# Kernel tuning notes

Hardware: AMD Instinct MI355X
Metric: run time of the kernel (lower is better)

Reference implementation:

```python
import jax, jax.numpy as jnp
import numpy as np

B, S, D = 2, 1024, 1024
H, KVH, HD = 16, 4, 64  # query heads, kv heads, head_dim
EPS = 1e-5
SCALE = float(np.sqrt(HD))  # note: scale uses original head_dim, not concat dim


def rmsnorm(x, g):
    return x * jax.lax.rsqrt(jnp.mean(x * x, axis=-1, keepdims=True) + EPS) * g


def rope(x, cos, sin):
    # x: [B,S,h,HD]; cos/sin: [S, HD//2]; pairs are consecutive (view_as_complex layout)
    xr = x.reshape(*x.shape[:-1], HD // 2, 2)
    x0, x1 = xr[..., 0], xr[..., 1]
    c = cos[None, :, None, :]
    s = sin[None, :, None, :]
    o0 = x0 * c - x1 * s
    o1 = x0 * s + x1 * c
    return jnp.stack([o0, o1], axis=-1).reshape(x.shape)


def context_build(x, W, gq, gk):
    comb = x @ W.T  # [B,S, H*HD + 2*KVH*HD]
    q, k, v = jnp.split(comb, [H * HD, H * HD + KVH * HD], axis=-1)
    q = rmsnorm(q, gq).reshape(B, S, H, HD)
    k = rmsnorm(k, gk).reshape(B, S, KVH, HD)
    v = v.reshape(B, S, KVH, HD)
    return q, k, v


def setup_inputs() -> dict:
    key = jax.random.key(0)
    ks = jax.random.split(key, 12)
    total = H * HD + 2 * KVH * HD  # 1536
    pos = jnp.arange(S, dtype=jnp.float32)
    theta = 10000.0 ** (-jnp.arange(0, HD, 2, dtype=jnp.float32) / HD)  # [HD//2]
    ang = pos[:, None] * theta[None, :]  # [S, HD//2]
    sc = 0.02
    return {
        "local_c": jax.random.normal(ks[0], (B, S, D), jnp.float32),
        "global_c": jax.random.normal(ks[1], (B, S, D), jnp.float32),
        "freqs_cos": jnp.cos(ang),
        "freqs_sin": jnp.sin(ang),
        "W_lc": jax.random.normal(ks[2], (total, D), jnp.float32) * sc,
        "W_gc": jax.random.normal(ks[3], (total, D), jnp.float32) * sc,
        "g_q_lc": jnp.ones((H * HD,), jnp.float32),
        "g_k_lc": jnp.ones((KVH * HD,), jnp.float32),
        "g_q_gc": jnp.ones((H * HD,), jnp.float32),
        "g_k_gc": jnp.ones((KVH * HD,), jnp.float32),
        "W_local": jax.random.normal(ks[4], (H * HD, 2 * H * HD), jnp.float32) * sc,
        "b_local": jnp.zeros((H * HD,), jnp.float32),
        "g_lc_out": jnp.ones((H * HD,), jnp.float32),
        "W_global": jax.random.normal(ks[5], (H * HD, 2 * H * HD), jnp.float32) * sc,
        "b_global": jnp.zeros((H * HD,), jnp.float32),
        "g_gc_out": jnp.ones((H * HD,), jnp.float32),
    }


def reference(local_c, global_c, freqs_cos, freqs_sin, W_lc, W_gc,
              g_q_lc, g_k_lc, g_q_gc, g_k_gc,
              W_local, b_local, g_lc_out, W_global, b_global, g_gc_out):
    q_lc, k_lc, v_lc = context_build(local_c, W_lc, g_q_lc, g_k_lc)
    q_gc, k_gc, v_gc = context_build(global_c, W_gc, g_q_gc, g_k_gc)

    q_lc = rope(q_lc, freqs_cos, freqs_sin)
    k_lc = rope(k_lc, freqs_cos, freqs_sin)
    q_gc = rope(q_gc, freqs_cos, freqs_sin)
    k_gc = rope(k_gc, freqs_cos, freqs_sin)

    # concat local+global along head_dim -> per-head dim 2*HD
    q = jnp.concatenate([q_lc, q_gc], axis=-1)  # [B,S,H,2HD]
    k = jnp.concatenate([k_lc, k_gc], axis=-1)  # [B,S,KVH,2HD]
    v = jnp.concatenate([v_lc, v_gc], axis=-1)

    n_rep = H // KVH
    k = jnp.repeat(k, n_rep, axis=2)  # [B,S,H,2HD] (GQA repeat_kv)
    v = jnp.repeat(v, n_rep, axis=2)

    scores = jnp.einsum("bqhd,bkhd->bhqk", q, k) / SCALE  # [B,H,S,S]
    attn = jax.nn.softmax(scores, axis=-1)
    out = jnp.einsum("bhqk,bkhd->bqhd", attn, v).reshape(B, S, H * 2 * HD)

    x_lc = rmsnorm(out @ W_local.T + b_local, g_lc_out)
    x_gc = rmsnorm(out @ W_global.T + b_global, g_gc_out)
    return (x_lc, x_gc)
```

## Files before the change

kernel.cpp:

```cpp
#include <hip/hip_runtime.h>

typedef __attribute__((ext_vector_type(8))) __bf16 bf16x8;
typedef __attribute__((ext_vector_type(4))) __bf16 bf16x4;
typedef __attribute__((ext_vector_type(4))) float f32x4;

__device__ __forceinline__ bf16x8 cvt8(const float* __restrict__ p)
{
    const float4 a = *(const float4*)p;
    const float4 b = *(const float4*)(p + 4);
    bf16x8 r;
    r[0] = (__bf16)a.x; r[1] = (__bf16)a.y; r[2] = (__bf16)a.z; r[3] = (__bf16)a.w;
    r[4] = (__bf16)b.x; r[5] = (__bf16)b.y; r[6] = (__bf16)b.z; r[7] = (__bf16)b.w;
    return r;
}

__device__ __forceinline__ void gld16(const __bf16* g, __bf16* l)
{
    __builtin_amdgcn_global_load_lds(
        (const __attribute__((address_space(1))) void*)g,
        (__attribute__((address_space(3))) void*)l, 16, 0, 0);
}

struct CvtArgs {
    const float* s[6];
    __bf16* d[6];
    int n[6];
};

__global__ __launch_bounds__(256) void cvt_bf16(CvtArgs a)
{
    const int t = blockIdx.y;
    const int i0 = (blockIdx.x * 256 + threadIdx.x) * 8;
    if (i0 < a.n[t])
        *(bf16x8*)(a.d[t] + i0) = cvt8(a.s[t] + i0);
}

template <typename CT>
__device__ __forceinline__ void gemm_core(const __bf16* __restrict__ Ap, int lda,
                                          const __bf16* __restrict__ Bp, int ldb,
                                          CT* __restrict__ Cp, int ldc, int K)
{
    __shared__ __bf16 As[2][128 * 32];
    __shared__ __bf16 Bs[2][128 * 32];
    const int tid  = threadIdx.x;
    const int w    = tid >> 6;
    const int lane = tid & 63;
    const int ln   = lane & 15;
    const int quad = lane >> 4;
    const int wm   = w & 1;
    const int wn   = w >> 1;

    const int srow = 32 * w + (lane >> 2);
    const int scol = (lane & 3) * 8;

    f32x4 acc[4][4];
    const f32x4 zero = {0.f, 0.f, 0.f, 0.f};
#pragma unroll
    for (int i = 0; i < 4; i++)
#pragma unroll
        for (int j = 0; j < 4; j++) acc[i][j] = zero;

    auto stage = [&](int buf, int k0) {
        gld16(Ap + (size_t)srow * lda        + k0 + scol, As[buf] + (2 * w)     * 512 + lane * 8);
        gld16(Ap + (size_t)(srow + 16) * lda + k0 + scol, As[buf] + (2 * w + 1) * 512 + lane * 8);
        gld16(Bp + (size_t)srow * ldb        + k0 + scol, Bs[buf] + (2 * w)     * 512 + lane * 8);
        gld16(Bp + (size_t)(srow + 16) * ldb + k0 + scol, Bs[buf] + (2 * w + 1) * 512 + lane * 8);
    };

    stage(0, 0);
    int buf = 0;
    for (int k0 = 0; k0 < K; k0 += 32, buf ^= 1) {
        __syncthreads();
        if (k0 + 32 < K) stage(buf ^ 1, k0 + 32);

        bf16x8 af[4], bw[4];
#pragma unroll
        for (int i = 0; i < 4; i++)
            af[i] = *(const bf16x8*)(As[buf] + (wm * 64 + i * 16 + ln) * 32 + quad * 8);
#pragma unroll
        for (int j = 0; j < 4; j++)
            bw[j] = *(const bf16x8*)(Bs[buf] + (wn * 64 + j * 16 + ln) * 32 + quad * 8);
#pragma unroll
        for (int i = 0; i < 4; i++)
#pragma unroll
            for (int j = 0; j < 4; j++)
                acc[i][j] = __builtin_amdgcn_mfma_f32_16x16x32_bf16(
                    af[i], bw[j], acc[i][j], 0, 0, 0);
    }

#pragma unroll
    for (int i = 0; i < 4; i++)
#pragma unroll
        for (int j = 0; j < 4; j++)
#pragma unroll
            for (int r = 0; r < 4; r++) {
                const int ml = wm * 64 + i * 16 + quad * 4 + r;
                const int nl = wn * 64 + j * 16 + ln;
                Cp[(size_t)ml * ldc + nl] = (CT)acc[i][j][r];
            }
}

__global__ __launch_bounds__(256) void gemm_qkv(const __bf16* __restrict__ Xbf,
                                                const __bf16* __restrict__ Wqkv,
                                                __bf16* __restrict__ comb)
{
    const int z = blockIdx.z;
    const __bf16* A = Xbf  + (size_t)z * 2048 * 1024 + (size_t)blockIdx.y * 128 * 1024;
    const __bf16* B = Wqkv + (size_t)z * 1536 * 1024 + (size_t)blockIdx.x * 128 * 1024;
    __bf16* C = comb + (size_t)z * 2048 * 1536 +
                (size_t)blockIdx.y * 128 * 1536 + (size_t)blockIdx.x * 128;
    gemm_core<__bf16>(A, 1024, B, 1024, C, 1536, 1024);
}

__global__ __launch_bounds__(256) void gemm_out(const __bf16* __restrict__ AO,
                                                const __bf16* __restrict__ Wout,
                                                __bf16* __restrict__ Y0,
                                                __bf16* __restrict__ Y1)
{
    const int kh = blockIdx.z;
    const __bf16* A = AO   + (size_t)blockIdx.y * 128 * 2048 + kh * 1024;
    const __bf16* B = Wout + (size_t)blockIdx.x * 128 * 2048 + kh * 1024;
    __bf16* Y = kh ? Y1 : Y0;
    __bf16* C = Y + (size_t)blockIdx.y * 128 * 2048 + (size_t)blockIdx.x * 128;
    gemm_core<__bf16>(A, 2048, B, 2048, C, 2048, 1024);
}

__global__ __launch_bounds__(256) void pack_qkv(
    const __bf16* __restrict__ comb,
    const float* __restrict__ fcos, const float* __restrict__ fsin,
    const float* __restrict__ g_q_lc, const float* __restrict__ g_k_lc,
    const float* __restrict__ g_q_gc, const float* __restrict__ g_k_gc,
    __bf16* __restrict__ Qb, __bf16* __restrict__ Kb, __bf16* __restrict__ Vb)
{
    const int m = blockIdx.x, ctx = blockIdx.y;
    const int b = m >> 10, s = m & 1023;
    const int tid = threadIdx.x;
    const __bf16* cr = comb + ((size_t)ctx * 2048 + m) * 1536;
    const float* gq = ctx ? g_q_gc : g_q_lc;
    const float* gk = ctx ? g_k_gc : g_k_lc;

    const bf16x4 qv = *(const bf16x4*)(cr + tid * 4);
    float sq = (float)qv[0] * (float)qv[0] + (float)qv[1] * (float)qv[1] +
               (float)qv[2] * (float)qv[2] + (float)qv[3] * (float)qv[3];
    const float kvv = (float)cr[1024 + tid];
    float sk = kvv * kvv;
#pragma unroll
    for (int off = 32; off > 0; off >>= 1) {
        sq += __shfl_down(sq, off);
        sk += __shfl_down(sk, off);
    }
    __shared__ float redq[4], redk[4];
    if ((tid & 63) == 0) { redq[tid >> 6] = sq; redk[tid >> 6] = sk; }
    __syncthreads();
    sq = redq[0] + redq[1] + redq[2] + redq[3];
    sk = redk[0] + redk[1] + redk[2] + redk[3];
    const float rq = rsqrtf(sq * (1.f / 1024.f) + 1e-5f);
    const float rk = rsqrtf(sk * (1.f / 256.f) + 1e-5f);

#pragma unroll
    for (int pp = 0; pp < 2; pp++) {
        const int p = tid + pp * 256;
        const int h = p >> 5, pi = p & 31;
        const float x0 = (float)cr[2 * p]     * rq * gq[2 * p];
        const float x1 = (float)cr[2 * p + 1] * rq * gq[2 * p + 1];
        const float c  = fcos[s * 32 + pi];
        const float sn = fsin[s * 32 + pi];
        const float o0 = (x0 * c - x1 * sn) * 0.125f;
        const float o1 = (x0 * sn + x1 * c) * 0.125f;
        const size_t qo = ((size_t)m * 16 + h) * 128 + ctx * 64 + 2 * pi;
        Qb[qo]     = (__bf16)o0;
        Qb[qo + 1] = (__bf16)o1;
    }
    if (tid < 128) {
        const int p = tid;
        const int kvh = p >> 5, pi = p & 31;
        const float x0 = (float)cr[1024 + 2 * p]     * rk * gk[2 * p];
        const float x1 = (float)cr[1024 + 2 * p + 1] * rk * gk[2 * p + 1];
        const float c  = fcos[s * 32 + pi];
        const float sn = fsin[s * 32 + pi];
        const float o0 = x0 * c - x1 * sn;
        const float o1 = x0 * sn + x1 * c;
        const size_t ko = ((size_t)(b * 4 + kvh) * 1024 + s) * 128 + ctx * 64 + 2 * pi;
        Kb[ko]     = (__bf16)o0;
        Kb[ko + 1] = (__bf16)o1;
    }
    {
        const int kvh = tid >> 6, d = tid & 63;
        Vb[((size_t)(b * 4 + kvh) * 1024 + s) * 128 + ctx * 64 + d] = cr[1280 + tid];
    }
}

__global__ __launch_bounds__(256) void v_transpose(const __bf16* __restrict__ Vb,
                                                   __bf16* __restrict__ Vtb)
{
    __shared__ __bf16 lds[64 * 64];
    const int st  = blockIdx.x;
    const int dt  = blockIdx.y;
    const int bkv = blockIdx.z;
    const int tid = threadIdx.x;
    const __bf16* src = Vb  + ((size_t)bkv * 1024 + st * 64) * 128 + dt * 64;
    __bf16*       dst = Vtb + ((size_t)bkv * 128 + dt * 64) * 1024 + st * 64;

#pragma unroll
    for (int i = 0; i < 2; i++) {
        const int c = tid + i * 256;
        const int s_in = c >> 3, ch = c & 7;
        const bf16x8 v = *(const bf16x8*)(src + (size_t)s_in * 128 + ch * 8);
        *(bf16x8*)&lds[s_in * 64 + (((ch + (s_in >> 3)) & 7) * 8)] = v;
    }
    __syncthreads();
#pragma unroll
    for (int i = 0; i < 2; i++) {
        const int c = tid + i * 256;
        const int dd = c >> 3, s0 = (c & 7) * 8;
        bf16x8 o;
#pragma unroll
        for (int jj = 0; jj < 8; jj++) {
            const int s = s0 + jj;
            o[jj] = lds[s * 64 + ((((dd >> 3) + (s >> 3)) & 7) * 8) + (dd & 7)];
        }
        *(bf16x8*)(dst + (size_t)dd * 1024 + s0) = o;
    }
}

__global__ __launch_bounds__(256) void attn(const __bf16* __restrict__ Qb,
                                            const __bf16* __restrict__ Kb,
                                            const __bf16* __restrict__ Vtb,
                                            __bf16* __restrict__ AO)
{
    __shared__ __bf16 Ks[2][64][136];
    __shared__ __bf16 Vts[2][128][72];
    __shared__ __bf16 Ps[4][16][72];

    const int tid  = threadIdx.x;
    const int w    = tid >> 6;
    const int lane = tid & 63;
    const int ln   = lane & 15;
    const int quad = lane >> 4;
    const int qt = blockIdx.x, h = blockIdx.y, b = blockIdx.z;
    const int kv = h >> 2;

    const __bf16* Kbase = Kb  + (size_t)(b * 4 + kv) * 1024 * 128;
    const __bf16* Vbase = Vtb + (size_t)(b * 4 + kv) * 128 * 1024;

    bf16x8 qf[4];
    const int qrow = qt * 64 + w * 16 + ln;
    const __bf16* qptr = Qb + ((size_t)(b * 1024 + qrow) * 16 + h) * 128;
#pragma unroll
    for (int kc = 0; kc < 4; kc++)
        qf[kc] = *(const bf16x8*)(qptr + kc * 32 + quad * 8);

    f32x4 oacc[8];
    const f32x4 zero = {0.f, 0.f, 0.f, 0.f};
#pragma unroll
    for (int j = 0; j < 8; j++) oacc[j] = zero;
    float lpart[4] = {0.f, 0.f, 0.f, 0.f};

    bf16x8 kreg[4], vreg[4];
    auto load_tiles = [&](int kt) {
        const int ks0 = kt * 64;
#pragma unroll
        for (int i = 0; i < 4; i++) {
            const int c = tid + i * 256;
            kreg[i] = *(const bf16x8*)(Kbase + (size_t)(ks0 + (c >> 4)) * 128 + (c & 15) * 8);
            vreg[i] = *(const bf16x8*)(Vbase + (size_t)(c >> 3) * 1024 + ks0 + (c & 7) * 8);
        }
    };
    auto write_tiles = [&](int buf) {
#pragma unroll
        for (int i = 0; i < 4; i++) {
            const int c = tid + i * 256;
            *(bf16x8*)&Ks[buf][c >> 4][(c & 15) * 8] = kreg[i];
            *(bf16x8*)&Vts[buf][c >> 3][(c & 7) * 8] = vreg[i];
        }
    };

    load_tiles(0);
    write_tiles(0);

    for (int kt = 0; kt < 16; kt++) {
        const int buf = kt & 1;
        if (kt + 1 < 16) load_tiles(kt + 1);
        __syncthreads();

        f32x4 sacc[4];
#pragma unroll
        for (int j = 0; j < 4; j++) {
            f32x4 a = zero;
#pragma unroll
            for (int kc = 0; kc < 4; kc++) {
                const bf16x8 kf =
                    *(const bf16x8*)&Ks[buf][j * 16 + ln][kc * 32 + quad * 8];
                a = __builtin_amdgcn_mfma_f32_16x16x32_bf16(qf[kc], kf, a, 0, 0, 0);
            }
            sacc[j] = a;
        }

#pragma unroll
        for (int j = 0; j < 4; j++)
#pragma unroll
            for (int r = 0; r < 4; r++) {
                const float p = __expf(sacc[j][r] - 20.f);
                lpart[r] += p;
                Ps[w][quad * 4 + r][j * 16 + ln] = (__bf16)p;
            }
#pragma unroll
        for (int kk = 0; kk < 2; kk++) {
            const bf16x8 pf = *(const bf16x8*)&Ps[w][ln][kk * 32 + quad * 8];
#pragma unroll
            for (int j2 = 0; j2 < 8; j2++) {
                const bf16x8 vf =
                    *(const bf16x8*)&Vts[buf][j2 * 16 + ln][kk * 32 + quad * 8];
                oacc[j2] = __builtin_amdgcn_mfma_f32_16x16x32_bf16(pf, vf, oacc[j2], 0, 0, 0);
            }
        }

        if (kt + 1 < 16) write_tiles(buf ^ 1);
    }

    float inv[4];
#pragma unroll
    for (int r = 0; r < 4; r++) {
        float rs = lpart[r];
#pragma unroll
        for (int off = 1; off < 16; off <<= 1)
            rs += __shfl_xor(rs, off);
        inv[r] = 1.f / rs;
    }
#pragma unroll
    for (int j2 = 0; j2 < 8; j2++)
#pragma unroll
        for (int r = 0; r < 4; r++) {
            const size_t row = (size_t)(b * 1024 + qt * 64 + w * 16 + quad * 4 + r);
            AO[row * 2048 + h * 128 + j2 * 16 + ln] = (__bf16)(oacc[j2][r] * inv[r]);
        }
}

__global__ __launch_bounds__(256) void rmsnorm_out(const __bf16* __restrict__ Y0,
                                                   const __bf16* __restrict__ Y1,
                                                   const float* __restrict__ b_l,
                                                   const float* __restrict__ b_g,
                                                   const float* __restrict__ g_l,
                                                   const float* __restrict__ g_g,
                                                   float* __restrict__ out)
{
    const int m = blockIdx.x, which = blockIdx.y;
    const int tid = threadIdx.x;
    const size_t off = (size_t)m * 2048 + which * 1024 + tid * 4;
    const float* bias = which ? b_g : b_l;
    const float* g    = which ? g_g : g_l;

    const bf16x4 y0 = *(const bf16x4*)(Y0 + off);
    const bf16x4 y1 = *(const bf16x4*)(Y1 + off);
    const float4 bv = *(const float4*)(bias + tid * 4);
    float x[4];
    x[0] = (float)y0[0] + (float)y1[0] + bv.x;
    x[1] = (float)y0[1] + (float)y1[1] + bv.y;
    x[2] = (float)y0[2] + (float)y1[2] + bv.z;
    x[3] = (float)y0[3] + (float)y1[3] + bv.w;
    float ss = x[0] * x[0] + x[1] * x[1] + x[2] * x[2] + x[3] * x[3];
#pragma unroll
    for (int off2 = 32; off2 > 0; off2 >>= 1) ss += __shfl_down(ss, off2);
    __shared__ float red[4];
    if ((tid & 63) == 0) red[tid >> 6] = ss;
    __syncthreads();
    ss = red[0] + red[1] + red[2] + red[3];
    const float r = rsqrtf(ss * (1.f / 1024.f) + 1e-5f);

    const float4 gv = *(const float4*)(g + tid * 4);
    float4 o;
    o.x = x[0] * r * gv.x;
    o.y = x[1] * r * gv.y;
    o.z = x[2] * r * gv.z;
    o.w = x[3] * r * gv.w;
    *(float4*)(out + (size_t)which * 2097152 + (size_t)m * 1024 + tid * 4) = o;
}

extern "C" void kernel_launch(void* const* d_in, const int* in_sizes, int n_in,
                              void* d_out, int out_size, void* d_ws, size_t ws_size,
                              hipStream_t stream)
{
    (void)in_sizes; (void)n_in; (void)out_size; (void)ws_size;
    const float* local_c  = (const float*)d_in[0];
    const float* global_c = (const float*)d_in[1];
    const float* fcos     = (const float*)d_in[2];
    const float* fsin     = (const float*)d_in[3];
    const float* W_lc     = (const float*)d_in[4];
    const float* W_gc     = (const float*)d_in[5];
    const float* g_q_lc   = (const float*)d_in[6];
    const float* g_k_lc   = (const float*)d_in[7];
    const float* g_q_gc   = (const float*)d_in[8];
    const float* g_k_gc   = (const float*)d_in[9];
    const float* W_local  = (const float*)d_in[10];
    const float* b_local  = (const float*)d_in[11];
    const float* g_lc_out = (const float*)d_in[12];
    const float* W_global = (const float*)d_in[13];
    const float* b_global = (const float*)d_in[14];
    const float* g_gc_out = (const float*)d_in[15];

    char* ws = (char*)d_ws;
    __bf16* Wout = (__bf16*)(ws + 0);
    __bf16* Xbf  = (__bf16*)(ws + 8388608);
    __bf16* Wqkv = (__bf16*)(ws + 16777216);
    __bf16* comb = (__bf16*)(ws + 23068672);
    __bf16* Qb   = (__bf16*)(ws + 35651584);
    __bf16* Kb   = (__bf16*)(ws + 44040192);
    __bf16* Vtb  = (__bf16*)(ws + 46137344);
    __bf16* AO   = (__bf16*)(ws + 48234496);
    __bf16* Y0   = (__bf16*)(ws + 56623104);
    __bf16* Y1   = (__bf16*)(ws + 65011712);
    __bf16* Vb   = (__bf16*)(ws + 56623104);

    CvtArgs ca;
    ca.s[0] = local_c;  ca.d[0] = Xbf;            ca.n[0] = 2097152;
    ca.s[1] = global_c; ca.d[1] = Xbf + 2097152;  ca.n[1] = 2097152;
    ca.s[2] = W_lc;     ca.d[2] = Wqkv;           ca.n[2] = 1572864;
    ca.s[3] = W_gc;     ca.d[3] = Wqkv + 1572864; ca.n[3] = 1572864;
    ca.s[4] = W_local;  ca.d[4] = Wout;           ca.n[4] = 2097152;
    ca.s[5] = W_global; ca.d[5] = Wout + 2097152; ca.n[5] = 2097152;

    cvt_bf16<<<dim3(1024, 6), 256, 0, stream>>>(ca);
    gemm_qkv<<<dim3(12, 16, 2), 256, 0, stream>>>(Xbf, Wqkv, comb);
    pack_qkv<<<dim3(2048, 2), 256, 0, stream>>>(comb, fcos, fsin,
                                                g_q_lc, g_k_lc, g_q_gc, g_k_gc,
                                                Qb, Kb, Vb);
    v_transpose<<<dim3(16, 2, 8), 256, 0, stream>>>(Vb, Vtb);
    attn<<<dim3(16, 16, 2), 256, 0, stream>>>(Qb, Kb, Vtb, AO);
    gemm_out<<<dim3(16, 16, 2), 256, 0, stream>>>(AO, Wout, Y0, Y1);
    rmsnorm_out<<<dim3(2048, 2), 256, 0, stream>>>(Y0, Y1, b_local, b_global,
                                                   g_lc_out, g_gc_out,
                                                   (float*)d_out);
}
```

Before: 213.3 us.

## Load K and V fragments directly from global memory in attention, drop LDS staging

Removes the double-buffered shared-memory K/V tiles and their block-wide barriers. Each wave now reads its MFMA K and V operands straight from global memory (relying on L1/L2 cache), and raises wave priority around the MFMA loops with s_setprio. This removes the LDS writes and syncs, but each of the four waves reloads the same K/V data, adding global-memory traffic and exposing load latency with no prefetching.

Result: slower. 303.2 us (+42.1%).

```diff
diff --git a/kernel.cpp b/kernel.cpp
--- a/kernel.cpp
+++ b/kernel.cpp
@@ -228,8 +228,6 @@
                                             const __bf16* __restrict__ Vtb,
                                             __bf16* __restrict__ AO)
 {
-    __shared__ __bf16 Ks[2][64][136];
-    __shared__ __bf16 Vts[2][128][72];
     __shared__ __bf16 Ps[4][16][72];
 
     const int tid  = threadIdx.x;
@@ -256,43 +254,21 @@
     for (int j = 0; j < 8; j++) oacc[j] = zero;
     float lpart[4] = {0.f, 0.f, 0.f, 0.f};
 
-    bf16x8 kreg[4], vreg[4];
-    auto load_tiles = [&](int kt) {
+    for (int kt = 0; kt < 16; kt++) {
         const int ks0 = kt * 64;
-#pragma unroll
-        for (int i = 0; i < 4; i++) {
-            const int c = tid + i * 256;
-            kreg[i] = *(const bf16x8*)(Kbase + (size_t)(ks0 + (c >> 4)) * 128 + (c & 15) * 8);
-            vreg[i] = *(const bf16x8*)(Vbase + (size_t)(c >> 3) * 1024 + ks0 + (c & 7) * 8);
-        }
-    };
-    auto write_tiles = [&](int buf) {
-#pragma unroll
-        for (int i = 0; i < 4; i++) {
-            const int c = tid + i * 256;
-            *(bf16x8*)&Ks[buf][c >> 4][(c & 15) * 8] = kreg[i];
-            *(bf16x8*)&Vts[buf][c >> 3][(c & 7) * 8] = vreg[i];
-        }
-    };
-
-    load_tiles(0);
-    write_tiles(0);
-
-    for (int kt = 0; kt < 16; kt++) {
-        const int buf = kt & 1;
-        if (kt + 1 < 16) load_tiles(kt + 1);
-        __syncthreads();
 
         f32x4 sacc[4];
 #pragma unroll
         for (int j = 0; j < 4; j++) {
+            const __bf16* kr = Kbase + (size_t)(ks0 + j * 16 + ln) * 128 + quad * 8;
             f32x4 a = zero;
+            __builtin_amdgcn_s_setprio(1);
 #pragma unroll
             for (int kc = 0; kc < 4; kc++) {
-                const bf16x8 kf =
-                    *(const bf16x8*)&Ks[buf][j * 16 + ln][kc * 32 + quad * 8];
+                const bf16x8 kf = *(const bf16x8*)(kr + kc * 32);
                 a = __builtin_amdgcn_mfma_f32_16x16x32_bf16(qf[kc], kf, a, 0, 0, 0);
             }
+            __builtin_amdgcn_s_setprio(0);
             sacc[j] = a;
         }
 
@@ -304,18 +280,19 @@
                 lpart[r] += p;
                 Ps[w][quad * 4 + r][j * 16 + ln] = (__bf16)p;
             }
+
 #pragma unroll
         for (int kk = 0; kk < 2; kk++) {
             const bf16x8 pf = *(const bf16x8*)&Ps[w][ln][kk * 32 + quad * 8];
+            const __bf16* vr = Vbase + (size_t)ln * 1024 + ks0 + kk * 32 + quad * 8;
+            __builtin_amdgcn_s_setprio(1);
 #pragma unroll
             for (int j2 = 0; j2 < 8; j2++) {
-                const bf16x8 vf =
-                    *(const bf16x8*)&Vts[buf][j2 * 16 + ln][kk * 32 + quad * 8];
+                const bf16x8 vf = *(const bf16x8*)(vr + (size_t)j2 * 16 * 1024);
                 oacc[j2] = __builtin_amdgcn_mfma_f32_16x16x32_bf16(pf, vf, oacc[j2], 0, 0, 0);
             }
+            __builtin_amdgcn_s_setprio(0);
         }
-
-        if (kt + 1 < 16) write_tiles(buf ^ 1);
     }
 
     float inv[4];
```
